# Performance work log

Measured on AMD Instinct MI355X. Metric: run time of the kernel, lower is better.

## Reference

```python
import jax, jax.numpy as jnp
import numpy as np

B, S, H = 2, 2048, 4096
NQ, NKV, D = 32, 8, 128
THETA = 10000.0


def setup_inputs() -> dict:
    key = jax.random.key(0)
    k0, k1, k2 = jax.random.split(key, 3)
    hidden_states = jax.random.normal(k0, (B, S, H), dtype=jnp.float32)
    w_qkv = jax.random.normal(k1, (H, (NQ + 2 * NKV) * D), dtype=jnp.float32) * 0.02
    w_o = jax.random.normal(k2, (NQ * D, H), dtype=jnp.float32) * 0.02
    positions = jnp.broadcast_to(jnp.arange(S, dtype=jnp.int32)[None, :], (B, S))
    return {"hidden_states": hidden_states, "w_qkv": w_qkv, "w_o": w_o,
            "positions": positions}


def _rope_gptj(x, cos, sin):
    # non-neox (GPT-J interleaved) RoPE; x: [B,S,h,D], cos/sin: [B,S,1,D/2]
    x1 = x[..., 0::2]
    x2 = x[..., 1::2]
    o1 = x1 * cos - x2 * sin
    o2 = x2 * cos + x1 * sin
    return jnp.stack([o1, o2], axis=-1).reshape(x.shape)


def reference(hidden_states, w_qkv, w_o, positions):
    scale = D ** -0.5
    qkv = hidden_states @ w_qkv  # [B,S,(NQ+2NKV)*D]
    q, k, v = jnp.split(qkv, [NQ * D, (NQ + NKV) * D], axis=-1)
    q = q.reshape(B, S, NQ, D)
    k = k.reshape(B, S, NKV, D)
    v = v.reshape(B, S, NKV, D)

    inv_freq = 1.0 / (THETA ** (jnp.arange(0, D, 2, dtype=jnp.float32) / D))
    freqs = positions.astype(jnp.float32)[..., None] * inv_freq  # [B,S,D/2]
    cos = jnp.cos(freqs)[:, :, None, :]
    sin = jnp.sin(freqs)[:, :, None, :]
    q = _rope_gptj(q, cos, sin)
    k = _rope_gptj(k, cos, sin)

    # GQA: expand kv heads to query heads
    rep = NQ // NKV
    k = jnp.repeat(k, rep, axis=2)  # [B,S,NQ,D]
    v = jnp.repeat(v, rep, axis=2)

    scores = jnp.einsum('bqhd,bkhd->bhqk', q, k) * scale
    causal = jnp.tril(jnp.ones((S, S), dtype=bool))
    scores = jnp.where(causal[None, None, :, :], scores, jnp.finfo(scores.dtype).min)
    probs = jax.nn.softmax(scores, axis=-1)
    attn = jnp.einsum('bhqk,bkhd->bqhd', probs, v).reshape(B, S, NQ * D)
    return attn @ w_o  # [B,S,H]
```

## Files before the change

kernel.cpp:

```cpp
#include <hip/hip_runtime.h>
#include <hip/hip_bf16.h>
#include <stdint.h>

#define B_  2
#define S_  2048
#define H_  4096
#define NQ_ 32
#define NKV_ 8
#define D_  128
#define NQKV_ 6144

typedef __bf16 bf16_t;
typedef __bf16 bf16x4 __attribute__((ext_vector_type(4)));
typedef __bf16 bf16x8 __attribute__((ext_vector_type(8)));
typedef float  floatx4 __attribute__((ext_vector_type(4)));

#define GLOBAL_AS __attribute__((address_space(1)))
#define LDS_AS    __attribute__((address_space(3)))

#define QSCALE (0.08838834764831845f * 1.4426950408889634f)

__global__ __launch_bounds__(256) void convert_f32_bf16(
    const float* __restrict__ src, bf16_t* __restrict__ dst, int n4) {
  int i = blockIdx.x * 256 + threadIdx.x;
  if (i < n4) {
    float4 v = ((const float4*)src)[i];
    bf16_t o[4] = {(bf16_t)v.x, (bf16_t)v.y, (bf16_t)v.z, (bf16_t)v.w};
    ((uint64_t*)dst)[i] = *(const uint64_t*)o;
  }
}

__global__ __launch_bounds__(256) void transpose_f32_bf16(
    const float* __restrict__ src, bf16_t* __restrict__ dst, int R, int C) {
  __shared__ bf16_t tile[64][65];
  const int ct = blockIdx.x * 64, rt = blockIdx.y * 64;
  const int t = threadIdx.x;
  const int cl = t & 63;
  for (int i = 0; i < 16; ++i) {
    int rl = i * 4 + (t >> 6);
    tile[rl][cl] = (bf16_t)src[(size_t)(rt + rl) * C + ct + cl];
  }
  __syncthreads();
  const int rl2 = t & 63;
  for (int i = 0; i < 16; ++i) {
    int cl2 = i * 4 + (t >> 6);
    dst[(size_t)(ct + cl2) * R + rt + rl2] = tile[rl2][cl2];
  }
}

template <typename OutT>
__global__ __launch_bounds__(512, 2) void gemm_abt256(
    const bf16_t* __restrict__ A, const bf16_t* __restrict__ Bt,
    OutT* __restrict__ C, int M, int N, int K) {
  __shared__ __align__(16) char lds[131072];

  const int nbx = gridDim.x;
  const int nwg = nbx * gridDim.y;
  int bid = blockIdx.y * nbx + blockIdx.x;
  bid = (bid & 7) * (nwg >> 3) + (bid >> 3);
  const int bx = bid % nbx, by = bid / nbx;

  const int tid = threadIdx.x;
  const int wave = tid >> 6, lane = tid & 63;
  const int lrow = lane & 15, quad = lane >> 4;
  const int wm = (wave >> 2) * 128;
  const int wn = (wave & 3) * 64;
  const int row0 = by * 256, col0 = bx * 256;

  const int lr = lane >> 3;
  const int lc = ((((lane & 7) << 4) ^ (lr << 4)) >> 1);

  auto stage = [&](int buf, int kt) {
    char* aB = lds + buf * 65536;
    char* bB = aB + 32768;
#pragma unroll
    for (int h = 0; h < 2; ++h)
#pragma unroll
      for (int i = 0; i < 2; ++i) {
        const bf16_t* ga =
            A + (size_t)(row0 + h * 128 + i * 64 + wave * 8 + lr) * K + kt + lc;
        __builtin_amdgcn_global_load_lds(
            (GLOBAL_AS void*)ga,
            (LDS_AS void*)(aB + h * 16384 + i * 8192 + wave * 1024), 16, 0, 0);
      }
#pragma unroll
    for (int h = 0; h < 2; ++h)
#pragma unroll
      for (int i = 0; i < 2; ++i) {
        const bf16_t* gb =
            Bt + (size_t)(col0 + h * 128 + i * 64 + wave * 8 + lr) * K + kt + lc;
        __builtin_amdgcn_global_load_lds(
            (GLOBAL_AS void*)gb,
            (LDS_AS void*)(bB + h * 16384 + i * 8192 + wave * 1024), 16, 0, 0);
      }
  };

  floatx4 acc[8][4] = {};
  const int nt = K >> 6;
  const int sw = (lrow & 7) << 4;

  stage(0, 0);
  int cur = 0;
  for (int t = 0; t < nt; ++t) {
    if (t + 1 < nt) stage(cur ^ 1, (t + 1) * 64);
    __builtin_amdgcn_sched_barrier(0);
    if (t + 1 < nt)
      asm volatile("s_waitcnt vmcnt(8)" ::: "memory");
    else
      asm volatile("s_waitcnt vmcnt(0)" ::: "memory");
    __builtin_amdgcn_s_barrier();
    __builtin_amdgcn_sched_barrier(0);

    const char* aB = lds + cur * 65536;
    const char* bB = aB + 32768;
    __builtin_amdgcn_s_setprio(1);
#pragma unroll
    for (int kk = 0; kk < 2; ++kk) {
      bf16x8 af[8], bfr[4];
#pragma unroll
      for (int fm = 0; fm < 8; ++fm) {
        const int r = wm + fm * 16 + lrow;
        af[fm] = *(const bf16x8*)(aB + r * 128 + ((kk * 64 + quad * 16) ^ sw));
      }
#pragma unroll
      for (int fn = 0; fn < 4; ++fn) {
        const int r = wn + fn * 16 + lrow;
        bfr[fn] = *(const bf16x8*)(bB + r * 128 + ((kk * 64 + quad * 16) ^ sw));
      }
#pragma unroll
      for (int fm = 0; fm < 8; ++fm)
#pragma unroll
        for (int fn = 0; fn < 4; ++fn)
          acc[fm][fn] = __builtin_amdgcn_mfma_f32_16x16x32_bf16(
              af[fm], bfr[fn], acc[fm][fn], 0, 0, 0);
    }
    __builtin_amdgcn_s_setprio(0);

    asm volatile("s_waitcnt lgkmcnt(0)" ::: "memory");
    __builtin_amdgcn_s_barrier();
    __builtin_amdgcn_sched_barrier(0);
    cur ^= 1;
  }

#pragma unroll
  for (int fm = 0; fm < 8; ++fm)
#pragma unroll
    for (int fn = 0; fn < 4; ++fn)
#pragma unroll
      for (int r = 0; r < 4; ++r) {
        int row = row0 + wm + fm * 16 + quad * 4 + r;
        int col = col0 + wn + fn * 16 + lrow;
        C[(size_t)row * N + col] = (OutT)acc[fm][fn][r];
      }
}

__global__ __launch_bounds__(256) void rope_qk(
    const bf16_t* __restrict__ qkv, const int* __restrict__ positions,
    bf16_t* __restrict__ Q, bf16_t* __restrict__ K) {
  const int row = blockIdx.x;
  const int b = row >> 11, s = row & (S_ - 1);
  const float pos = (float)positions[row];
  const bf16_t* src = qkv + (size_t)row * NQKV_;
  for (int p = threadIdx.x; p < (NQ_ + NKV_) * 64; p += 256) {
    const int head = p >> 6, i = p & 63;
    const float inv = __powf(10000.0f, -(float)i * (1.0f / 64.0f));
    const float f = pos * inv;
    const float cs = __cosf(f), sn = __sinf(f);
    const float x1 = (float)src[head * 128 + 2 * i];
    const float x2 = (float)src[head * 128 + 2 * i + 1];
    float o1 = x1 * cs - x2 * sn;
    float o2 = x2 * cs + x1 * sn;
    bf16_t* dst;
    if (head < NQ_) {
      o1 *= QSCALE;
      o2 *= QSCALE;
      dst = Q + ((size_t)(b * NQ_ + head) * S_ + s) * D_ + 2 * i;
    } else {
      dst = K + ((size_t)(b * NKV_ + (head - NQ_)) * S_ + s) * D_ + 2 * i;
    }
    dst[0] = (bf16_t)o1;
    dst[1] = (bf16_t)o2;
  }
}

__global__ __launch_bounds__(256) void v_transpose(
    const bf16_t* __restrict__ qkv, bf16_t* __restrict__ Vt) {
  __shared__ bf16_t tile[64][65];
  const int b = blockIdx.z;
  const int kh = blockIdx.y >> 1;
  const int dt = (blockIdx.y & 1) * 64;
  const int st = blockIdx.x * 64;
  const int t = threadIdx.x;
  const int colbase = (NQ_ + NKV_) * D_ + kh * D_ + dt;
  for (int i = 0; i < 16; ++i) {
    int sl = i * 4 + (t >> 6);
    int dl = t & 63;
    tile[sl][dl] = qkv[(size_t)(b * S_ + st + sl) * NQKV_ + colbase + dl];
  }
  __syncthreads();
  for (int i = 0; i < 16; ++i) {
    int dl = i * 4 + (t >> 6);
    int sl = t & 63;
    Vt[((size_t)(b * NKV_ + kh) * D_ + dt + dl) * S_ + st + sl] = tile[sl][dl];
  }
}

__global__ __launch_bounds__(256) void flash_attn(
    const bf16_t* __restrict__ Q, const bf16_t* __restrict__ K,
    const bf16_t* __restrict__ Vt, bf16_t* __restrict__ O) {
  const int qt = (S_ / 64 - 1) - blockIdx.x;
  const int h  = blockIdx.y;
  const int b  = blockIdx.z;
  const int kh = h >> 2;
  const int tid = threadIdx.x, wave = tid >> 6, lane = tid & 63;
  const int lrow = lane & 15, quad = lane >> 4;
  const int q0 = qt * 64;

  __shared__ __align__(16) char lKb[64 * 256];
  __shared__ __align__(16) char lVb[128 * 128];
  __shared__ __align__(16) char lPb[64 * 128];

#define LK(r, c) (lKb + ((r) << 8) + ((c) ^ (((r) & 7) << 4)))
#define LV(r, c) (lVb + ((r) << 7) + ((c) ^ (((r) & 7) << 4)))
#define LP(r, c) (lPb + ((r) << 7) + ((c) ^ (((r) & 7) << 4)))

  const bf16_t* Qbase = Q  + ((size_t)(b * NQ_ + h) * S_) * D_;
  const bf16_t* Kbase = K  + ((size_t)(b * NKV_ + kh) * S_) * D_;
  const bf16_t* Vbase = Vt + ((size_t)(b * NKV_ + kh) * D_) * S_;

  const int qrow = q0 + wave * 16 + lrow;
  bf16x8 qf[4];
  {
    const bf16_t* qp = Qbase + (size_t)qrow * D_ + quad * 8;
    for (int ks = 0; ks < 4; ++ks) qf[ks] = *(const bf16x8*)(qp + ks * 32);
  }

  const int krow = tid >> 4;
  const int kcol = ((((tid & 15) << 4)) ^ ((krow & 7) << 4)) >> 1;
  const int vrow = tid >> 3;
  const int vcol = ((((tid & 7) << 4)) ^ ((vrow & 7) << 4)) >> 1;

  floatx4 acc[8] = {};
  float mrun = -3.0e38f, lrun = 0.0f;

  const int nkt = qt + 1;
  for (int kt = 0; kt < nkt; ++kt) {
    const int k0 = kt * 64;
    __syncthreads();
#pragma unroll
    for (int i = 0; i < 4; ++i) {
      const bf16_t* ga = Kbase + (size_t)(k0 + i * 16 + krow) * D_ + kcol;
      __builtin_amdgcn_global_load_lds((GLOBAL_AS void*)ga,
          (LDS_AS void*)(lKb + i * 4096 + wave * 1024), 16, 0, 0);
    }
#pragma unroll
    for (int i = 0; i < 4; ++i) {
      const bf16_t* ga = Vbase + (size_t)(i * 32 + vrow) * S_ + k0 + vcol;
      __builtin_amdgcn_global_load_lds((GLOBAL_AS void*)ga,
          (LDS_AS void*)(lVb + i * 4096 + wave * 1024), 16, 0, 0);
    }
    __syncthreads();

    floatx4 sacc[4];
#pragma unroll
    for (int t = 0; t < 4; ++t) {
      floatx4 a = {0.f, 0.f, 0.f, 0.f};
#pragma unroll
      for (int ks = 0; ks < 4; ++ks) {
        bf16x8 kf = *(const bf16x8*)LK(t * 16 + lrow, ks * 64 + quad * 16);
        a = __builtin_amdgcn_mfma_f32_16x16x32_bf16(kf, qf[ks], a, 0, 0, 0);
      }
      sacc[t] = a;
    }

    if (kt == qt) {
#pragma unroll
      for (int t = 0; t < 4; ++t)
#pragma unroll
        for (int r = 0; r < 4; ++r) {
          const int kpos = k0 + t * 16 + quad * 4 + r;
          if (kpos > qrow) sacc[t][r] = -3.0e38f;
        }
    }

    float mx = -3.0e38f;
#pragma unroll
    for (int t = 0; t < 4; ++t)
#pragma unroll
      for (int r = 0; r < 4; ++r) mx = fmaxf(mx, sacc[t][r]);
    mx = fmaxf(mx, __shfl_xor(mx, 16));
    mx = fmaxf(mx, __shfl_xor(mx, 32));

    float mcur = mrun;
    if (!__all(mx - mrun <= 8.0f)) {
      const float mnew = fmaxf(mrun, mx);
      const float alpha = exp2f(mrun - mnew);
      lrun *= alpha;
#pragma unroll
      for (int dt = 0; dt < 8; ++dt) acc[dt] *= alpha;
      mrun = mnew;
      mcur = mnew;
    }

    float rs = 0.0f;
#pragma unroll
    for (int t = 0; t < 4; ++t) {
      bf16x4 pk;
#pragma unroll
      for (int r = 0; r < 4; ++r) {
        float p = exp2f(sacc[t][r] - mcur);
        rs += p;
        pk[r] = (bf16_t)p;
      }
      *(bf16x4*)LP(wave * 16 + lrow, t * 32 + quad * 8) = pk;
    }
    rs += __shfl_xor(rs, 16);
    rs += __shfl_xor(rs, 32);
    lrun += rs;

    bf16x8 pf0 = *(const bf16x8*)LP(wave * 16 + lrow, quad * 16);
    bf16x8 pf1 = *(const bf16x8*)LP(wave * 16 + lrow, 64 + quad * 16);
#pragma unroll
    for (int dt = 0; dt < 8; ++dt) {
      bf16x8 v0 = *(const bf16x8*)LV(dt * 16 + lrow, quad * 16);
      bf16x8 v1 = *(const bf16x8*)LV(dt * 16 + lrow, 64 + quad * 16);
      floatx4 a = acc[dt];
      a = __builtin_amdgcn_mfma_f32_16x16x32_bf16(v0, pf0, a, 0, 0, 0);
      a = __builtin_amdgcn_mfma_f32_16x16x32_bf16(v1, pf1, a, 0, 0, 0);
      acc[dt] = a;
    }
  }

  const float inv_l = 1.0f / lrun;
  bf16_t* Obase = O + ((size_t)(b * S_) + qrow) * (NQ_ * D_) + h * D_;
#pragma unroll
  for (int dt = 0; dt < 8; ++dt) {
    bf16x4 ov;
#pragma unroll
    for (int r = 0; r < 4; ++r) ov[r] = (bf16_t)(acc[dt][r] * inv_l);
    *(bf16x4*)(Obase + dt * 16 + quad * 4) = ov;
  }
#undef LK
#undef LV
#undef LP
}

extern "C" void kernel_launch(void* const* d_in, const int* in_sizes, int n_in,
                              void* d_out, int out_size, void* d_ws, size_t ws_size,
                              hipStream_t stream) {
  const float* hs    = (const float*)d_in[0];
  const float* w_qkv = (const float*)d_in[1];
  const float* w_o   = (const float*)d_in[2];
  const int*   pos   = (const int*)d_in[3];
  float* out = (float*)d_out;

  char* ws = (char*)d_ws;
  constexpr size_t OFF_WT  = 0;
  constexpr size_t OFF_QKV = 50331648;
  constexpr size_t OFF_Q   = OFF_QKV + 50331648;
  constexpr size_t OFF_K   = OFF_Q + 33554432;
  constexpr size_t OFF_VT  = OFF_K + 8388608;
  bf16_t* wT    = (bf16_t*)(ws + OFF_WT);
  bf16_t* qkv   = (bf16_t*)(ws + OFF_QKV);
  bf16_t* Qb    = (bf16_t*)(ws + OFF_Q);
  bf16_t* Kb    = (bf16_t*)(ws + OFF_K);
  bf16_t* Vtb   = (bf16_t*)(ws + OFF_VT);
  bf16_t* hsb   = Qb;
  bf16_t* attnO = qkv;

  convert_f32_bf16<<<dim3((B_ * S_ * H_ / 4) / 256), 256, 0, stream>>>(
      hs, hsb, B_ * S_ * H_ / 4);
  transpose_f32_bf16<<<dim3(NQKV_ / 64, H_ / 64), 256, 0, stream>>>(
      w_qkv, wT, H_, NQKV_);
  gemm_abt256<bf16_t><<<dim3(NQKV_ / 256, (B_ * S_) / 256), 512, 0, stream>>>(
      hsb, wT, qkv, B_ * S_, NQKV_, H_);
  rope_qk<<<dim3(B_ * S_), 256, 0, stream>>>(qkv, pos, Qb, Kb);
  v_transpose<<<dim3(S_ / 64, NKV_ * 2, B_), 256, 0, stream>>>(qkv, Vtb);
  transpose_f32_bf16<<<dim3(H_ / 64, (NQ_ * D_) / 64), 256, 0, stream>>>(
      w_o, wT, NQ_ * D_, H_);
  flash_attn<<<dim3(S_ / 64, NQ_, B_), 256, 0, stream>>>(Qb, Kb, Vtb, attnO);
  gemm_abt256<float><<<dim3(H_ / 256, (B_ * S_) / 256), 512, 0, stream>>>(
      attnO, wT, out, B_ * S_, H_, H_);

  (void)in_sizes; (void)n_in; (void)out_size; (void)ws_size;
}
```

Before: 827.1 us.

## Split GEMM tile into four quadrant phases with staggered half-tile prefetch

Restructures the 256x256 bf16 GEMM main loop into four compute phases, one per 128x128 quadrant of A/B halves. Each phase issues the prefetch of one half-tile for the next k-step and waits only on the half-tile it needs, which interleaves global-to-LDS loads with MFMA work instead of staging everything up front and waiting on one barrier. The wave-to-output mapping changes so each wave owns a 64x32 piece of every quadrant. The cost is more barriers per k-step and more delicate vmcnt bookkeeping, which could stall or race if the counts are wrong.

```diff
diff --git a/kernel.cpp b/kernel.cpp
--- a/kernel.cpp
+++ b/kernel.cpp
@@ -63,95 +63,115 @@
   const int tid = threadIdx.x;
   const int wave = tid >> 6, lane = tid & 63;
   const int lrow = lane & 15, quad = lane >> 4;
-  const int wm = (wave >> 2) * 128;
-  const int wn = (wave & 3) * 64;
+  const int wr = wave >> 2, wc = wave & 3;
   const int row0 = by * 256, col0 = bx * 256;
 
   const int lr = lane >> 3;
   const int lc = ((((lane & 7) << 4) ^ (lr << 4)) >> 1);
 
-  auto stage = [&](int buf, int kt) {
-    char* aB = lds + buf * 65536;
-    char* bB = aB + 32768;
-#pragma unroll
-    for (int h = 0; h < 2; ++h)
-#pragma unroll
-      for (int i = 0; i < 2; ++i) {
-        const bf16_t* ga =
-            A + (size_t)(row0 + h * 128 + i * 64 + wave * 8 + lr) * K + kt + lc;
-        __builtin_amdgcn_global_load_lds(
-            (GLOBAL_AS void*)ga,
-            (LDS_AS void*)(aB + h * 16384 + i * 8192 + wave * 1024), 16, 0, 0);
-      }
-#pragma unroll
-    for (int h = 0; h < 2; ++h)
-#pragma unroll
-      for (int i = 0; i < 2; ++i) {
-        const bf16_t* gb =
-            Bt + (size_t)(col0 + h * 128 + i * 64 + wave * 8 + lr) * K + kt + lc;
-        __builtin_amdgcn_global_load_lds(
-            (GLOBAL_AS void*)gb,
-            (LDS_AS void*)(bB + h * 16384 + i * 8192 + wave * 1024), 16, 0, 0);
-      }
+  auto stageHalf = [&](char* dst, const bf16_t* src, int grow, int kt) {
+#pragma unroll
+    for (int i = 0; i < 2; ++i) {
+      const bf16_t* g =
+          src + (size_t)(grow + i * 64 + wave * 8 + lr) * K + kt + lc;
+      __builtin_amdgcn_global_load_lds((GLOBAL_AS void*)g,
+          (LDS_AS void*)(dst + i * 8192 + wave * 1024), 16, 0, 0);
+    }
   };
 
-  floatx4 acc[8][4] = {};
+  floatx4 acc[2][2][4][2] = {};
   const int nt = K >> 6;
   const int sw = (lrow & 7) << 4;
 
-  stage(0, 0);
-  int cur = 0;
+#define PHASE_COMPUTE(MH, NH)                                               \
+  {                                                                         \
+    bf16x8 af[4][2], bfr[2][2];                                             \
+    _Pragma("unroll") for (int fm = 0; fm < 4; ++fm) {                      \
+      const int rh = wr * 64 + fm * 16 + lrow;                              \
+      _Pragma("unroll") for (int kk = 0; kk < 2; ++kk)                      \
+        af[fm][kk] = *(const bf16x8*)(aB + (MH) * 16384 + rh * 128 +        \
+                                      ((kk * 64 + quad * 16) ^ sw));        \
+    }                                                                       \
+    _Pragma("unroll") for (int fn = 0; fn < 2; ++fn) {                      \
+      const int rb = wc * 32 + fn * 16 + lrow;                              \
+      _Pragma("unroll") for (int kk = 0; kk < 2; ++kk)                      \
+        bfr[fn][kk] = *(const bf16x8*)(bB + (NH) * 16384 + rb * 128 +       \
+                                       ((kk * 64 + quad * 16) ^ sw));       \
+    }                                                                       \
+    __builtin_amdgcn_s_setprio(1);                                          \
+    _Pragma("unroll") for (int kk = 0; kk < 2; ++kk)                        \
+      _Pragma("unroll") for (int fm = 0; fm < 4; ++fm)                      \
+        _Pragma("unroll") for (int fn = 0; fn < 2; ++fn)                    \
+          acc[MH][NH][fm][fn] = __builtin_amdgcn_mfma_f32_16x16x32_bf16(    \
+              af[fm][kk], bfr[fn][kk], acc[MH][NH][fm][fn], 0, 0, 0);       \
+    __builtin_amdgcn_s_setprio(0);                                          \
+  }
+
+#define PIN() __builtin_amdgcn_sched_barrier(0)
+
+  stageHalf(lds + 0,     A,  row0,       0);
+  stageHalf(lds + 32768, Bt, col0,       0);
+  stageHalf(lds + 16384, A,  row0 + 128, 0);
+  stageHalf(lds + 49152, Bt, col0 + 128, 0);
+
   for (int t = 0; t < nt; ++t) {
-    if (t + 1 < nt) stage(cur ^ 1, (t + 1) * 64);
-    __builtin_amdgcn_sched_barrier(0);
-    if (t + 1 < nt)
-      asm volatile("s_waitcnt vmcnt(8)" ::: "memory");
-    else
-      asm volatile("s_waitcnt vmcnt(0)" ::: "memory");
-    __builtin_amdgcn_s_barrier();
-    __builtin_amdgcn_sched_barrier(0);
-
+    const int cur = t & 1;
     const char* aB = lds + cur * 65536;
     const char* bB = aB + 32768;
-    __builtin_amdgcn_s_setprio(1);
-#pragma unroll
-    for (int kk = 0; kk < 2; ++kk) {
-      bf16x8 af[8], bfr[4];
-#pragma unroll
-      for (int fm = 0; fm < 8; ++fm) {
-        const int r = wm + fm * 16 + lrow;
-        af[fm] = *(const bf16x8*)(aB + r * 128 + ((kk * 64 + quad * 16) ^ sw));
-      }
-#pragma unroll
-      for (int fn = 0; fn < 4; ++fn) {
-        const int r = wn + fn * 16 + lrow;
-        bfr[fn] = *(const bf16x8*)(bB + r * 128 + ((kk * 64 + quad * 16) ^ sw));
-      }
-#pragma unroll
-      for (int fm = 0; fm < 8; ++fm)
-#pragma unroll
-        for (int fn = 0; fn < 4; ++fn)
-          acc[fm][fn] = __builtin_amdgcn_mfma_f32_16x16x32_bf16(
-              af[fm], bfr[fn], acc[fm][fn], 0, 0, 0);
-    }
-    __builtin_amdgcn_s_setprio(0);
-
-    asm volatile("s_waitcnt lgkmcnt(0)" ::: "memory");
+    char* aS = lds + (cur ^ 1) * 65536;
+    char* bS = aS + 32768;
+    const int kt1 = (t + 1) * 64;
+    const bool pf = (t + 1 < nt);
+
+    PIN();
+    asm volatile("s_waitcnt vmcnt(4)" ::: "memory");
+    PIN();
     __builtin_amdgcn_s_barrier();
-    __builtin_amdgcn_sched_barrier(0);
-    cur ^= 1;
-  }
-
-#pragma unroll
-  for (int fm = 0; fm < 8; ++fm)
-#pragma unroll
-    for (int fn = 0; fn < 4; ++fn)
-#pragma unroll
-      for (int r = 0; r < 4; ++r) {
-        int row = row0 + wm + fm * 16 + quad * 4 + r;
-        int col = col0 + wn + fn * 16 + lrow;
-        C[(size_t)row * N + col] = (OutT)acc[fm][fn][r];
-      }
+    PIN();
+    if (pf) stageHalf(aS, A, row0, kt1);
+    PHASE_COMPUTE(0, 0)
+
+    PIN();
+    if (pf) asm volatile("s_waitcnt vmcnt(4)" ::: "memory");
+    else    asm volatile("s_waitcnt vmcnt(2)" ::: "memory");
+    PIN();
+    __builtin_amdgcn_s_barrier();
+    PIN();
+    if (pf) stageHalf(bS, Bt, col0, kt1);
+    PHASE_COMPUTE(1, 0)
+
+    PIN();
+    if (pf) asm volatile("s_waitcnt vmcnt(4)" ::: "memory");
+    else    asm volatile("s_waitcnt vmcnt(0)" ::: "memory");
+    PIN();
+    __builtin_amdgcn_s_barrier();
+    PIN();
+    if (pf) stageHalf(aS + 16384, A, row0 + 128, kt1);
+    PHASE_COMPUTE(0, 1)
+
+    PIN();
+    __builtin_amdgcn_s_barrier();
+    PIN();
+    if (pf) stageHalf(bS + 16384, Bt, col0 + 128, kt1);
+    PHASE_COMPUTE(1, 1)
+  }
+
+#pragma unroll
+  for (int mh = 0; mh < 2; ++mh)
+#pragma unroll
+    for (int nh = 0; nh < 2; ++nh)
+#pragma unroll
+      for (int fm = 0; fm < 4; ++fm)
+#pragma unroll
+        for (int fn = 0; fn < 2; ++fn)
+#pragma unroll
+          for (int r = 0; r < 4; ++r) {
+            int row = row0 + mh * 128 + wr * 64 + fm * 16 + quad * 4 + r;
+            int col = col0 + nh * 128 + wc * 32 + fn * 16 + lrow;
+            C[(size_t)row * N + col] = (OutT)acc[mh][nh][fm][fn][r];
+          }
+#undef PHASE_COMPUTE
+#undef PIN
 }
 
 __global__ __launch_bounds__(256) void rope_qk(
```

Measured after the change: 841.2 us. Within noise of the previous version (+1.7%).
